# Kernel optimization log

Measured on AMD Instinct MI355X. Metric: run time of the kernel, lower is better.

## Reference

```python
import jax, jax.numpy as jnp
import numpy as np


def setup_inputs() -> dict:
    key = jax.random.key(0)
    k1, k2, k3, k4, k5 = jax.random.split(key, 5)
    B, C, H, W = 2, 3, 64, 64
    f_tar = jax.random.normal(k1, (B, C, H, W), dtype=jnp.float32)
    f_src = jax.random.normal(k2, (B, C, H, W), dtype=jnp.float32)
    # Pinhole intrinsics (focal=50, principal point at image center) + small noise,
    # guaranteed invertible.
    K_base = jnp.array([[50.0, 0.0, 32.0], [0.0, 50.0, 32.0], [0.0, 0.0, 1.0]],
                       dtype=jnp.float32)
    K = K_base[None] + 0.05 * jax.random.normal(k3, (B, 3, 3), dtype=jnp.float32)
    # Near-identity rotation-like matrix.
    R = jnp.eye(3, dtype=jnp.float32)[None] + 0.1 * jax.random.normal(
        k4, (B, 3, 3), dtype=jnp.float32)
    t = jax.random.normal(k5, (B, 3, 1), dtype=jnp.float32)
    return {"f_tar": f_tar, "f_src": f_src, "K": K, "R": R, "t": t}


def reference(f_tar, f_src, K, R, t):
    B, C, H, W = f_src.shape  # C == 3 (required by the cross product)
    N = H * W
    dtype = f_src.dtype

    f_src_flat = f_src.reshape(B, C, N)  # (B, 3, N)
    f_tar_flat = f_tar.reshape(B, C, N)  # (B, 3, N)

    # A[b, i, j] = <f_src[:, i], f_tar[:, j]>  -> (B, N, N)
    A = jnp.einsum('bci,bcj->bij', f_src_flat, f_tar_flat)

    # Homogeneous pixel coordinates (3, N): rows of meshgrid(H, W, indexing='ij').
    ix, iy = jnp.meshgrid(jnp.arange(H), jnp.arange(W), indexing='ij')
    pix = jnp.stack([ix.reshape(-1), iy.reshape(-1), jnp.ones(N, dtype=jnp.int32)],
                    axis=0).astype(dtype)  # (3, N)

    K_inv = jnp.linalg.inv(K)  # (B, 3, 3)
    # tar_proj = K @ (R @ (K^-1 @ x) + t)   -> (B, 3, N)
    cam_rays = jnp.einsum('bij,jn->bin', K_inv, pix)
    tar_proj = jnp.einsum('bij,bjn->bin', K, jnp.einsum('bij,bjn->bin', R, cam_rays) + t)
    # Origin projects to K @ (R @ 0 + t) = K @ t, broadcast over N.
    o_proj = jnp.einsum('bij,bjn->bin', K, t)  # (B, 3, 1)

    diff = tar_proj - o_proj  # (B, 3, N)

    # Epipolar distance: || (f_src - o) x diff || / ||diff||, broadcast to (B, N, N).
    a = f_src_flat[:, :, :, None] - o_proj[:, :, :, None]  # (B, 3, N, 1)
    b = diff[:, :, None, :]                                 # (B, 3, 1, N)
    cross = jnp.cross(a, b, axis=1)                         # (B, 3, N, N)
    cross_norm = jnp.linalg.norm(cross, axis=1)             # (B, N, N)
    diff_norm = jnp.linalg.norm(diff, axis=1, keepdims=True)  # (B, 1, N)
    d_epipolar = cross_norm / diff_norm                     # (B, N, N)

    # 'sigmoid' in the original is nn.Softmax(dim=-1).
    EPI_THRESH = 0.5
    SHARPNESS = 50.0
    weight_map = 1.0 - jax.nn.softmax(SHARPNESS * (d_epipolar - EPI_THRESH), axis=-1)

    A_weighted = A * weight_map
    attention_map = jax.nn.softmax(A_weighted, axis=1)  # normalize over src positions

    # (B, N, N) @ (B, N, C) -> (B, N, C), then raw view back to (B, C, H, W)
    attended = jnp.einsum('bik,bck->bic', attention_map, f_src_flat)
    return attended.reshape(B, C, H, W)
```

## Files before the change

kernel.cpp:

```cpp
#include <hip/hip_runtime.h>
#include <hip/hip_bf16.h>

namespace {
constexpr int BB = 2;
constexpr int NN = 4096;

constexpr int OFF_SRC4 = 0;
constexpr int OFF_TAR4 = 4 * BB * NN;
constexpr int OFF_U4   = 8 * BB * NN;
constexpr int OFF_W4   = 12 * BB * NN;
constexpr int OFF_ROW  = 16 * BB * NN;
constexpr int OFF_CS   = 18 * BB * NN;
constexpr int OFF_NMAX = 19 * BB * NN;
constexpr size_t OFF_EB = (size_t)1 << 20;
constexpr float L2E = 1.4426950408889634f;
constexpr float S50 = 72.13475204444817f;
constexpr float BIAS = 10.0f;
}

__device__ __forceinline__ float fsqrt(float x) { return __builtin_amdgcn_sqrtf(x); }
__device__ __forceinline__ float ex2(float x) { return __builtin_amdgcn_exp2f(x); }

__global__ __launch_bounds__(256) void k_setup(
    const float* __restrict__ fsrc, const float* __restrict__ ftar,
    const float* __restrict__ Kb, const float* __restrict__ Rb,
    const float* __restrict__ tb, float* __restrict__ ws) {
  int gid = blockIdx.x * blockDim.x + threadIdx.x;
  if (gid >= BB * NN) return;
  int b = gid >> 12;
  int n = gid & (NN - 1);

  float K[9], R[9], t3[3];
#pragma unroll
  for (int k = 0; k < 9; k++) { K[k] = Kb[b * 9 + k]; R[k] = Rb[b * 9 + k]; }
#pragma unroll
  for (int k = 0; k < 3; k++) t3[k] = tb[b * 3 + k];

  float c00 = K[4] * K[8] - K[5] * K[7];
  float c01 = K[5] * K[6] - K[3] * K[8];
  float c02 = K[3] * K[7] - K[4] * K[6];
  float det = K[0] * c00 + K[1] * c01 + K[2] * c02;
  float id = 1.0f / det;
  float Ki[9];
  Ki[0] = c00 * id; Ki[1] = (K[2] * K[7] - K[1] * K[8]) * id; Ki[2] = (K[1] * K[5] - K[2] * K[4]) * id;
  Ki[3] = c01 * id; Ki[4] = (K[0] * K[8] - K[2] * K[6]) * id; Ki[5] = (K[2] * K[3] - K[0] * K[5]) * id;
  Ki[6] = c02 * id; Ki[7] = (K[1] * K[6] - K[0] * K[7]) * id; Ki[8] = (K[0] * K[4] - K[1] * K[3]) * id;

  float RK[9];
#pragma unroll
  for (int i = 0; i < 3; i++)
#pragma unroll
    for (int j = 0; j < 3; j++)
      RK[i * 3 + j] = R[i * 3 + 0] * Ki[j] + R[i * 3 + 1] * Ki[3 + j] + R[i * 3 + 2] * Ki[6 + j];
  float M3[9];
#pragma unroll
  for (int i = 0; i < 3; i++)
#pragma unroll
    for (int j = 0; j < 3; j++)
      M3[i * 3 + j] = K[i * 3 + 0] * RK[j] + K[i * 3 + 1] * RK[3 + j] + K[i * 3 + 2] * RK[6 + j];
  float o0 = K[0] * t3[0] + K[1] * t3[1] + K[2] * t3[2];
  float o1 = K[3] * t3[0] + K[4] * t3[1] + K[5] * t3[2];
  float o2 = K[6] * t3[0] + K[7] * t3[1] + K[8] * t3[2];

  float sx = fsrc[b * 3 * NN + 0 * NN + n];
  float sy = fsrc[b * 3 * NN + 1 * NN + n];
  float sz = fsrc[b * 3 * NN + 2 * NN + n];
  float tx = ftar[b * 3 * NN + 0 * NN + n];
  float ty = ftar[b * 3 * NN + 1 * NN + n];
  float tz = ftar[b * 3 * NN + 2 * NN + n];

  float ux = sx - o0, uy = sy - o1, uz = sz - o2;
  float usq = ux * ux + uy * uy + uz * uz;

  float px = (float)(n >> 6), py = (float)(n & 63);
  float vx = M3[0] * px + M3[1] * py + M3[2];
  float vy = M3[3] * px + M3[4] * py + M3[5];
  float vz = M3[6] * px + M3[7] * py + M3[8];
  float invn = rsqrtf(vx * vx + vy * vy + vz * vz);

  float4* src4 = (float4*)(ws + OFF_SRC4);
  float4* tar4 = (float4*)(ws + OFF_TAR4);
  float4* u4 = (float4*)(ws + OFF_U4);
  float4* w4 = (float4*)(ws + OFF_W4);
  src4[gid] = make_float4(sx, sy, sz, 0.f);
  tar4[gid] = make_float4(tx, ty, tz, 0.f);
  u4[gid] = make_float4(ux, uy, uz, usq);
  w4[gid] = make_float4(vx * invn, vy * invn, vz * invn, 0.f);

  float ns = fsqrt(sx * sx + sy * sy + sz * sz);
#pragma unroll
  for (int off = 32; off; off >>= 1) ns = fmaxf(ns, __shfl_xor(ns, off));
  if ((threadIdx.x & 63) == 0)
    atomicMax((unsigned int*)(ws + OFF_NMAX + b), __float_as_uint(ns));
}

__global__ __launch_bounds__(256, 4) void k_pass1(float* __restrict__ ws) {
  __shared__ float sred[4][8];
  const float4* u4 = (const float4*)(ws + OFF_U4);
  const float4* w4 = (const float4*)(ws + OFF_W4);
  float2* rowst = (float2*)(ws + OFF_ROW);
  int tid = threadIdx.x, wid = tid >> 6, lane = tid & 63;
  int g0 = blockIdx.x * 8;
  int b = g0 >> 12;

  float ux[8], uy[8], uz[8], us[8];
#pragma unroll
  for (int r = 0; r < 8; r++) {
    float4 u = u4[g0 + r];
    ux[r] = u.x; uy[r] = u.y; uz[r] = u.z; us[r] = u.w;
  }
  const float4* wb = w4 + b * NN;

  float mx[8] = {0.f, 0.f, 0.f, 0.f, 0.f, 0.f, 0.f, 0.f};
  for (int j = wid * 64 + lane; j < NN; j += 256) {
    float4 w = wb[j];
#pragma unroll
    for (int r = 0; r < 8; r++) {
      float dot = ux[r] * w.x + uy[r] * w.y + uz[r] * w.z;
      mx[r] = fmaxf(mx[r], us[r] - dot * dot);
    }
  }
#pragma unroll
  for (int off = 32; off; off >>= 1)
#pragma unroll
    for (int r = 0; r < 8; r++) mx[r] = fmaxf(mx[r], __shfl_xor(mx[r], off));
  if (lane == 0) {
#pragma unroll
    for (int r = 0; r < 8; r++) sred[wid][r] = mx[r];
  }
  __syncthreads();
  float m2[8];
#pragma unroll
  for (int r = 0; r < 8; r++)
    m2[r] = S50 * fsqrt(fmaxf(fmaxf(sred[0][r], sred[1][r]), fmaxf(sred[2][r], sred[3][r])));
  __syncthreads();

  float s[8] = {0.f, 0.f, 0.f, 0.f, 0.f, 0.f, 0.f, 0.f};
  for (int j = wid * 64 + lane; j < NN; j += 256) {
    float4 w = wb[j];
#pragma unroll
    for (int r = 0; r < 8; r++) {
      float dot = ux[r] * w.x + uy[r] * w.y + uz[r] * w.z;
      float d2 = fmaxf(us[r] - dot * dot, 0.f);
      float t = fsqrt(d2);
      s[r] += ex2(fmaf(S50, t, -m2[r]));
    }
  }
#pragma unroll
  for (int off = 32; off; off >>= 1)
#pragma unroll
    for (int r = 0; r < 8; r++) s[r] += __shfl_xor(s[r], off);
  if (lane == 0) {
#pragma unroll
    for (int r = 0; r < 8; r++) sred[wid][r] = s[r];
  }
  __syncthreads();
  if (tid < 8) {
    float tot = sred[0][tid] + sred[1][tid] + sred[2][tid] + sred[3][tid];
    rowst[g0 + tid] = make_float2(m2[tid], 1.f / tot);
  }
}

__global__ __launch_bounds__(256, 4) void k_pass2(float* __restrict__ ws) {
  __shared__ float sS[4][8];
  const float4* u4 = (const float4*)(ws + OFF_U4);
  const float4* w4 = (const float4*)(ws + OFF_W4);
  const float4* src4 = (const float4*)(ws + OFF_SRC4);
  const float4* tar4 = (const float4*)(ws + OFF_TAR4);
  const float2* rowst = (const float2*)(ws + OFF_ROW);
  float* CS = ws + OFF_CS;
  _Float16* Eh = (_Float16*)((char*)ws + OFF_EB);

  int tid = threadIdx.x, wid = tid >> 6, lane = tid & 63;
  int c0 = blockIdx.x * 8;
  int b = c0 >> 12;
  int base = b * NN;
  float maxns = ws[OFF_NMAX + b];

  float wx[8], wy[8], wz[8], txl[8], tyl[8], tzl[8], Cj[8];
#pragma unroll
  for (int r = 0; r < 8; r++) {
    float4 w = w4[c0 + r];
    float4 tt = tar4[c0 + r];
    wx[r] = w.x; wy[r] = w.y; wz[r] = w.z;
    txl[r] = tt.x * L2E; tyl[r] = tt.y * L2E; tzl[r] = tt.z * L2E;
    Cj[r] = BIAS - maxns * L2E * fsqrt(tt.x * tt.x + tt.y * tt.y + tt.z * tt.z);
  }

  float S[8] = {0.f, 0.f, 0.f, 0.f, 0.f, 0.f, 0.f, 0.f};
  for (int i = wid * 64 + lane; i < NN; i += 256) {
    float4 uv = u4[base + i];
    float4 sv = src4[base + i];
    float2 rs = rowst[base + i];
#pragma unroll
    for (int r = 0; r < 8; r++) {
      float dot = uv.x * wx[r] + uv.y * wy[r] + uv.z * wz[r];
      float d2 = fmaxf(uv.w - dot * dot, 0.f);
      float t = fsqrt(d2);
      float ev = ex2(fmaf(S50, t, -rs.x));
      float wgt = fmaf(-ev, rs.y, 1.f);
      float Ap = sv.x * txl[r] + sv.y * tyl[r] + sv.z * tzl[r];
      float Ev = ex2(fmaf(Ap, wgt, Cj[r]));
      S[r] += Ev;
      Eh[(size_t)(c0 + r) * NN + i] = (_Float16)Ev;
    }
  }
#pragma unroll
  for (int off = 32; off; off >>= 1)
#pragma unroll
    for (int r = 0; r < 8; r++) S[r] += __shfl_xor(S[r], off);
  if (lane == 0) {
#pragma unroll
    for (int r = 0; r < 8; r++) sS[wid][r] = S[r];
  }
  __syncthreads();
  if (tid < 8) {
    float tot = sS[0][tid] + sS[1][tid] + sS[2][tid] + sS[3][tid];
    CS[c0 + tid] = 1.f / tot;
  }
}

__global__ __launch_bounds__(256, 4) void k_pass3(const float* __restrict__ ws,
                                                  float* __restrict__ out) {
  __shared__ float4 ssrc[512];
  __shared__ float sinv[512];
  __shared__ float smrg[4][64][3];
  const float4* src4 = (const float4*)(ws + OFF_SRC4);
  const float* CS = ws + OFF_CS;
  const _Float16* Eh = (const _Float16*)((const char*)ws + OFF_EB);

  int tid = threadIdx.x, wid = tid >> 6, lane = tid & 63;
  int g = blockIdx.x >> 3;
  int c = blockIdx.x & 7;
  int b = g >> 6;
  int base = b * NN;
  int i_loc = (g & 63) * 64 + lane;
  int j0 = c * 512;

  ssrc[tid] = src4[base + j0 + tid];
  ssrc[tid + 256] = src4[base + j0 + 256 + tid];
  sinv[tid] = CS[base + j0 + tid];
  sinv[tid + 256] = CS[base + j0 + 256 + tid];
  __syncthreads();

  float a0 = 0.f, a1 = 0.f, a2 = 0.f;
  const _Float16* Ep = Eh + ((size_t)(base + j0 + wid * 128)) * NN + i_loc;
#pragma unroll 4
  for (int jj = 0; jj < 128; ++jj) {
    int jl = wid * 128 + jj;
    float4 sj = ssrc[jl];
    float p = (float)Ep[(size_t)jj * NN] * sinv[jl];
    a0 = fmaf(p, sj.x, a0);
    a1 = fmaf(p, sj.y, a1);
    a2 = fmaf(p, sj.z, a2);
  }
  smrg[wid][lane][0] = a0;
  smrg[wid][lane][1] = a1;
  smrg[wid][lane][2] = a2;
  __syncthreads();
  if (wid == 0) {
    float v0 = smrg[0][lane][0] + smrg[1][lane][0] + smrg[2][lane][0] + smrg[3][lane][0];
    float v1 = smrg[0][lane][1] + smrg[1][lane][1] + smrg[2][lane][1] + smrg[3][lane][1];
    float v2 = smrg[0][lane][2] + smrg[1][lane][2] + smrg[2][lane][2] + smrg[3][lane][2];
    int o = (base + i_loc) * 3;
    atomicAdd(&out[o + 0], v0);
    atomicAdd(&out[o + 1], v1);
    atomicAdd(&out[o + 2], v2);
  }
}

extern "C" void kernel_launch(void* const* d_in, const int* in_sizes, int n_in,
                              void* d_out, int out_size, void* d_ws, size_t ws_size,
                              hipStream_t stream) {
  (void)in_sizes; (void)n_in; (void)ws_size;
  const float* ftar = (const float*)d_in[0];
  const float* fsrc = (const float*)d_in[1];
  const float* K = (const float*)d_in[2];
  const float* R = (const float*)d_in[3];
  const float* t = (const float*)d_in[4];
  float* ws = (float*)d_ws;
  float* out = (float*)d_out;

  hipMemsetAsync((char*)d_ws + (size_t)OFF_NMAX * sizeof(float), 0, BB * sizeof(float), stream);
  hipMemsetAsync(d_out, 0, (size_t)out_size * sizeof(float), stream);

  k_setup<<<dim3((BB * NN + 255) / 256), dim3(256), 0, stream>>>(fsrc, ftar, K, R, t, ws);
  k_pass1<<<dim3(1024), dim3(256), 0, stream>>>(ws);
  k_pass2<<<dim3(1024), dim3(256), 0, stream>>>(ws);
  k_pass3<<<dim3(1024), dim3(256), 0, stream>>>(ws, out);
}
```

Measured before the change: 140.7 us.

## Skip negligible epipolar exp terms and vectorize pass3 fp16 loads

```diff
diff --git a/kernel.cpp b/kernel.cpp
--- a/kernel.cpp
+++ b/kernel.cpp
@@ -15,8 +15,12 @@
 constexpr size_t OFF_EB = (size_t)1 << 20;
 constexpr float L2E = 1.4426950408889634f;
 constexpr float S50 = 72.13475204444817f;
+constexpr float INV_S50 = 0.013862943611198906f;
 constexpr float BIAS = 10.0f;
-}
+constexpr float SKIP = 30.0f;
+}
+
+typedef _Float16 h2 __attribute__((ext_vector_type(2)));
 
 __device__ __forceinline__ float fsqrt(float x) { return __builtin_amdgcn_sqrtf(x); }
 __device__ __forceinline__ float ex2(float x) { return __builtin_amdgcn_exp2f(x); }
@@ -77,15 +81,17 @@
   float vy = M3[3] * px + M3[4] * py + M3[5];
   float vz = M3[6] * px + M3[7] * py + M3[8];
   float invn = rsqrtf(vx * vx + vy * vy + vz * vz);
+  float wxn = vx * invn, wyn = vy * invn, wzn = vz * invn;
+  float ow = o0 * wxn + o1 * wyn + o2 * wzn;
 
   float4* src4 = (float4*)(ws + OFF_SRC4);
   float4* tar4 = (float4*)(ws + OFF_TAR4);
   float4* u4 = (float4*)(ws + OFF_U4);
   float4* w4 = (float4*)(ws + OFF_W4);
-  src4[gid] = make_float4(sx, sy, sz, 0.f);
+  src4[gid] = make_float4(sx, sy, sz, usq);
   tar4[gid] = make_float4(tx, ty, tz, 0.f);
   u4[gid] = make_float4(ux, uy, uz, usq);
-  w4[gid] = make_float4(vx * invn, vy * invn, vz * invn, 0.f);
+  w4[gid] = make_float4(wxn, wyn, wzn, ow);
 
   float ns = fsqrt(sx * sx + sy * sy + sz * sz);
 #pragma unroll
@@ -129,21 +135,32 @@
     for (int r = 0; r < 8; r++) sred[wid][r] = mx[r];
   }
   __syncthreads();
-  float m2[8];
-#pragma unroll
-  for (int r = 0; r < 8; r++)
+  float m2[8], thr2[8];
+#pragma unroll
+  for (int r = 0; r < 8; r++) {
     m2[r] = S50 * fsqrt(fmaxf(fmaxf(sred[0][r], sred[1][r]), fmaxf(sred[2][r], sred[3][r])));
+    float thr = (m2[r] - SKIP) * INV_S50;
+    thr2[r] = (m2[r] > SKIP) ? thr * thr : -1.0f;
+  }
   __syncthreads();
 
   float s[8] = {0.f, 0.f, 0.f, 0.f, 0.f, 0.f, 0.f, 0.f};
   for (int j = wid * 64 + lane; j < NN; j += 256) {
     float4 w = wb[j];
+    float d2v[8];
+    int full = 0;
 #pragma unroll
     for (int r = 0; r < 8; r++) {
       float dot = ux[r] * w.x + uy[r] * w.y + uz[r] * w.z;
-      float d2 = fmaxf(us[r] - dot * dot, 0.f);
-      float t = fsqrt(d2);
-      s[r] += ex2(fmaf(S50, t, -m2[r]));
+      d2v[r] = fmaf(-dot, dot, us[r]);
+      full |= (d2v[r] >= thr2[r]) ? 1 : 0;
+    }
+    if (__any(full)) {
+#pragma unroll
+      for (int r = 0; r < 8; r++) {
+        float t = fsqrt(fmaxf(d2v[r], 0.f));
+        s[r] += ex2(fmaf(S50, t, -m2[r]));
+      }
     }
   }
 #pragma unroll
@@ -163,7 +180,6 @@
 
 __global__ __launch_bounds__(256, 4) void k_pass2(float* __restrict__ ws) {
   __shared__ float sS[4][8];
-  const float4* u4 = (const float4*)(ws + OFF_U4);
   const float4* w4 = (const float4*)(ws + OFF_W4);
   const float4* src4 = (const float4*)(ws + OFF_SRC4);
   const float4* tar4 = (const float4*)(ws + OFF_TAR4);
@@ -177,32 +193,36 @@
   int base = b * NN;
   float maxns = ws[OFF_NMAX + b];
 
-  float wx[8], wy[8], wz[8], txl[8], tyl[8], tzl[8], Cj[8];
+  float wx[8], wy[8], wz[8], now[8], txl[8], tyl[8], tzl[8], Cj[8];
 #pragma unroll
   for (int r = 0; r < 8; r++) {
     float4 w = w4[c0 + r];
     float4 tt = tar4[c0 + r];
-    wx[r] = w.x; wy[r] = w.y; wz[r] = w.z;
+    wx[r] = w.x; wy[r] = w.y; wz[r] = w.z; now[r] = -w.w;
     txl[r] = tt.x * L2E; tyl[r] = tt.y * L2E; tzl[r] = tt.z * L2E;
     Cj[r] = BIAS - maxns * L2E * fsqrt(tt.x * tt.x + tt.y * tt.y + tt.z * tt.z);
   }
 
   float S[8] = {0.f, 0.f, 0.f, 0.f, 0.f, 0.f, 0.f, 0.f};
   for (int i = wid * 64 + lane; i < NN; i += 256) {
-    float4 uv = u4[base + i];
     float4 sv = src4[base + i];
     float2 rs = rowst[base + i];
+    float thr = (rs.x - SKIP) * INV_S50;
+    float thr2 = (rs.x > SKIP) ? thr * thr : -1.0f;
 #pragma unroll
     for (int r = 0; r < 8; r++) {
-      float dot = uv.x * wx[r] + uv.y * wy[r] + uv.z * wz[r];
-      float d2 = fmaxf(uv.w - dot * dot, 0.f);
-      float t = fsqrt(d2);
-      float ev = ex2(fmaf(S50, t, -rs.x));
-      float wgt = fmaf(-ev, rs.y, 1.f);
-      float Ap = sv.x * txl[r] + sv.y * tyl[r] + sv.z * tzl[r];
+      float dot = fmaf(sv.x, wx[r], fmaf(sv.y, wy[r], fmaf(sv.z, wz[r], now[r])));
+      float d2 = fmaf(-dot, dot, sv.w);
+      float Ap = fmaf(sv.x, txl[r], fmaf(sv.y, tyl[r], sv.z * tzl[r]));
+      float wgt = 1.0f;
+      if (__any(d2 >= thr2)) {
+        float t = fsqrt(fmaxf(d2, 0.f));
+        float ev = ex2(fmaf(S50, t, -rs.x));
+        wgt = fmaf(-ev, rs.y, 1.f);
+      }
       float Ev = ex2(fmaf(Ap, wgt, Cj[r]));
       S[r] += Ev;
-      Eh[(size_t)(c0 + r) * NN + i] = (_Float16)Ev;
+      __builtin_nontemporal_store((_Float16)Ev, &Eh[(size_t)(c0 + r) * NN + i]);
     }
   }
 #pragma unroll
@@ -222,50 +242,51 @@
 
 __global__ __launch_bounds__(256, 4) void k_pass3(const float* __restrict__ ws,
                                                   float* __restrict__ out) {
-  __shared__ float4 ssrc[512];
-  __shared__ float sinv[512];
-  __shared__ float smrg[4][64][3];
+  __shared__ float4 ssrc[256];
+  __shared__ float sinv[256];
+  __shared__ float smrg[4][128][3];
   const float4* src4 = (const float4*)(ws + OFF_SRC4);
   const float* CS = ws + OFF_CS;
   const _Float16* Eh = (const _Float16*)((const char*)ws + OFF_EB);
 
   int tid = threadIdx.x, wid = tid >> 6, lane = tid & 63;
-  int g = blockIdx.x >> 3;
-  int c = blockIdx.x & 7;
-  int b = g >> 6;
+  int g = blockIdx.x >> 4;
+  int c = blockIdx.x & 15;
+  int b = g >> 5;
   int base = b * NN;
-  int i_loc = (g & 63) * 64 + lane;
-  int j0 = c * 512;
+  int i0 = (g & 31) * 128 + lane * 2;
+  int j0 = c * 256;
 
   ssrc[tid] = src4[base + j0 + tid];
-  ssrc[tid + 256] = src4[base + j0 + 256 + tid];
   sinv[tid] = CS[base + j0 + tid];
-  sinv[tid + 256] = CS[base + j0 + 256 + tid];
-  __syncthreads();
-
-  float a0 = 0.f, a1 = 0.f, a2 = 0.f;
-  const _Float16* Ep = Eh + ((size_t)(base + j0 + wid * 128)) * NN + i_loc;
+  __syncthreads();
+
+  float a00 = 0.f, a01 = 0.f, a02 = 0.f, a10 = 0.f, a11 = 0.f, a12 = 0.f;
 #pragma unroll 4
-  for (int jj = 0; jj < 128; ++jj) {
-    int jl = wid * 128 + jj;
+  for (int jj = 0; jj < 64; ++jj) {
+    int jl = wid * 64 + jj;
     float4 sj = ssrc[jl];
-    float p = (float)Ep[(size_t)jj * NN] * sinv[jl];
-    a0 = fmaf(p, sj.x, a0);
-    a1 = fmaf(p, sj.y, a1);
-    a2 = fmaf(p, sj.z, a2);
-  }
-  smrg[wid][lane][0] = a0;
-  smrg[wid][lane][1] = a1;
-  smrg[wid][lane][2] = a2;
-  __syncthreads();
-  if (wid == 0) {
-    float v0 = smrg[0][lane][0] + smrg[1][lane][0] + smrg[2][lane][0] + smrg[3][lane][0];
-    float v1 = smrg[0][lane][1] + smrg[1][lane][1] + smrg[2][lane][1] + smrg[3][lane][1];
-    float v2 = smrg[0][lane][2] + smrg[1][lane][2] + smrg[2][lane][2] + smrg[3][lane][2];
-    int o = (base + i_loc) * 3;
-    atomicAdd(&out[o + 0], v0);
-    atomicAdd(&out[o + 1], v1);
-    atomicAdd(&out[o + 2], v2);
+    float iv = sinv[jl];
+    h2 e2 = *(const h2*)&Eh[(size_t)(base + j0 + jl) * NN + i0];
+    float p0 = (float)e2.x * iv;
+    float p1 = (float)e2.y * iv;
+    a00 = fmaf(p0, sj.x, a00); a01 = fmaf(p0, sj.y, a01); a02 = fmaf(p0, sj.z, a02);
+    a10 = fmaf(p1, sj.x, a10); a11 = fmaf(p1, sj.y, a11); a12 = fmaf(p1, sj.z, a12);
+  }
+  smrg[wid][lane * 2 + 0][0] = a00;
+  smrg[wid][lane * 2 + 0][1] = a01;
+  smrg[wid][lane * 2 + 0][2] = a02;
+  smrg[wid][lane * 2 + 1][0] = a10;
+  smrg[wid][lane * 2 + 1][1] = a11;
+  smrg[wid][lane * 2 + 1][2] = a12;
+  __syncthreads();
+  if (tid < 128) {
+    int gi = base + (g & 31) * 128 + tid;
+#pragma unroll
+    for (int cc = 0; cc < 3; cc++) {
+      float v = smrg[0][tid][cc] + smrg[1][tid][cc] + smrg[2][tid][cc] + smrg[3][tid][cc];
+      atomicAdd(&out[gi * 3 + cc], v);
+    }
   }
 }
 
```

New measurement: 135.0 us. -4.1%, faster.
